# Performance work log

Hardware: AMD Instinct MI355X
Metric: run time of the kernel (lower is better)

The kernel has to match this reference:

```python
import jax, jax.numpy as jnp
import numpy as np

V, D, S, B, NL = 32000, 512, 1024, 2, 2
DS, KC, DI, DFF, E, TOPK = 16, 4, 1024, 2048, 8, 2
EPS = 1e-6


def rmsnorm(x, w):
    return x * jax.lax.rsqrt(jnp.mean(x * x, -1, keepdims=True) + EPS) * w


def mamba(x, in_w, conv_w, conv_b, x_proj_w, dt_w, dt_b, A_log, out_w):
    # x: (B, S, D)
    Bb, L, _ = x.shape
    xz = x @ in_w.T                      # (B, S, 2*DI)
    xi, z = jnp.split(xz, 2, axis=-1)    # each (B, S, DI)
    # causal depthwise conv (pad k-1 left == torch pad k-1 both + trim to L)
    xc = jnp.swapaxes(xi, 1, 2)          # (B, DI, S)
    xc = jax.lax.conv_general_dilated(
        xc, conv_w, window_strides=(1,), padding=[(KC - 1, 0)],
        dimension_numbers=("NCH", "OIH", "NCH"), feature_group_count=DI)
    xi = jnp.swapaxes(xc + conv_b[None, :, None], 1, 2)  # (B, S, DI)
    x_dbl = xi @ x_proj_w.T              # (B, S, 2*DS)
    B_param = x_dbl[..., DS:]            # (B, S, DS); first chunk overwritten in source
    delta = jax.nn.softplus(xi @ dt_w.T + dt_b)          # (B, S, DS)
    A = -jnp.exp(A_log)                  # (DI, DS)
    # recurrence coefficients (state dim summed out, as in source)
    a = jnp.exp(delta[:, :, None, :] * A[None, None]).sum(-1)        # (B, S, DI)
    b = xi * (delta * B_param).sum(-1, keepdims=True)                # (B, S, DI)

    def step(y, ab):
        at, bt = ab
        y = at * y + bt
        return y, y

    _, ys = jax.lax.scan(step, jnp.zeros((Bb, DI), x.dtype),
                         (jnp.swapaxes(a, 0, 1), jnp.swapaxes(b, 0, 1)))
    y = jnp.swapaxes(ys, 0, 1)           # (B, S, DI)
    y = y * jax.nn.silu(z)
    return y @ out_w.T                   # (B, S, D)


def moe(x, rw, rb, w1, b1, w2, b2):
    router_logits = x @ rw.T + rb                     # (B, S, E)
    probs = jax.nn.softmax(router_logits, axis=-1)
    topv, topi = jax.lax.top_k(probs, TOPK)
    wts = topv / topv.sum(-1, keepdims=True)          # renormalized gates
    h = jax.nn.gelu(jnp.einsum("bsd,efd->bsef", x, w1) + b1)   # (B, S, E, DFF)
    eo = jnp.einsum("bsef,edf->bsed", h, w2) + b2               # (B, S, E, D)
    sel = jnp.take_along_axis(eo, topi[..., None], axis=2)      # (B, S, K, D)
    out = (wts[..., None] * sel).sum(2)
    # load-balancing aux loss
    f = jax.nn.one_hot(topi, E).sum(2).mean((0, 1)) / TOPK
    P = probs.mean((0, 1))
    aux = E * jnp.sum(f * P)
    return out, aux


def setup_inputs() -> dict:
    key = jax.random.key(0)
    ks = jax.random.split(key, 16)
    f = lambda k, s: jax.random.normal(k, s, dtype=jnp.float32) * 0.02
    return {
        "input_ids": jax.random.randint(ks[0], (B, S), 0, V),
        "tok_emb": f(ks[1], (V, D)),
        "pos_emb": f(ks[2], (S, D)),
        "norm1_w": jnp.ones((NL, D), jnp.float32),
        "norm2_w": jnp.ones((NL, D), jnp.float32),
        "in_proj_w": f(ks[3], (NL, 2 * DI, D)),
        "conv_w": f(ks[4], (NL, DI, 1, KC)),
        "conv_b": jnp.zeros((NL, DI), jnp.float32),
        "x_proj_w": f(ks[5], (NL, 2 * DS, DI)),
        "dt_proj_w": f(ks[6], (NL, DS, DI)),
        "dt_proj_b": jnp.zeros((NL, DS), jnp.float32),
        "A_log": jnp.tile(jnp.log(jnp.arange(1, DS + 1, dtype=jnp.float32)), (NL, DI, 1)),
        "D_param": jnp.ones((NL, DI), jnp.float32),  # unused in forward, as in source
        "out_proj_w": f(ks[7], (NL, D, DI)),
        "router_w": f(ks[8], (NL, E, D)),
        "router_b": jnp.zeros((NL, E), jnp.float32),
        "w1": f(ks[9], (NL, E, DFF, D)),
        "b1": jnp.zeros((NL, E, DFF), jnp.float32),
        "w2": f(ks[10], (NL, E, D, DFF)),
        "b2": jnp.zeros((NL, E, D), jnp.float32),
        "final_norm_w": jnp.ones((D,), jnp.float32),
        "lm_head_w": f(ks[11], (V, D)),
    }


def reference(input_ids, tok_emb, pos_emb, norm1_w, norm2_w, in_proj_w, conv_w,
              conv_b, x_proj_w, dt_proj_w, dt_proj_b, A_log, D_param, out_proj_w,
              router_w, router_b, w1, b1, w2, b2, final_norm_w, lm_head_w):
    x = tok_emb[input_ids] + pos_emb[None, :, :]
    aux_total = jnp.zeros((), x.dtype)
    for l in range(NL):
        m = mamba(rmsnorm(x, norm1_w[l]), in_proj_w[l], conv_w[l], conv_b[l],
                  x_proj_w[l], dt_proj_w[l], dt_proj_b[l], A_log[l], out_proj_w[l])
        x = x + m
        ff, aux = moe(rmsnorm(x, norm2_w[l]), router_w[l], router_b[l],
                      w1[l], b1[l], w2[l], b2[l])
        x = x + ff
        aux_total = aux_total + aux
    x = rmsnorm(x, final_norm_w)
    logits = x @ lm_head_w.T
    return logits, aux_total
```

## Files before the change

kernel.cpp:

```cpp
#include <hip/hip_runtime.h>
#include <math.h>

#define S_    1024
#define D_    512
#define DI_   1024
#define DS_   16
#define KC_   4
#define E_    8
#define DFF_  2048
#define NTOK  2048
#define VOCAB 32000
#define NCHUNK 16
#define CHL    64
#define NSLOT 4096

typedef unsigned short ushort;
typedef unsigned int   uint;
typedef __attribute__((ext_vector_type(8))) short short8;
typedef __attribute__((ext_vector_type(4))) float f32x4;

__device__ __forceinline__ float gelu_sig(float x){
  float u = x*(1.5957691216057308f + 0.07135481627f*x*x);
  return x / (1.0f + expf(-u));
}
__device__ __forceinline__ ushort f2bf_rnd(float f){
  uint u = __float_as_uint(f);
  return (ushort)((u + 0x8000u) >> 16);
}
__device__ __forceinline__ float bf2f(ushort h){
  return __uint_as_float(((uint)h) << 16);
}
__device__ __forceinline__ void split1(float f, ushort& h, ushort& l){
  h = f2bf_rnd(f);
  float fh = bf2f(h);
  l = (ushort)(__float_as_uint(f - fh) >> 16);
}

__global__ __launch_bounds__(128) void k_embed(const int* __restrict__ ids,
    const float* __restrict__ tok, const float* __restrict__ pos, float* __restrict__ x){
  int t  = blockIdx.x;
  int d4 = threadIdx.x << 2;
  int s  = t & (S_-1);
  int id = ids[t];
  float4 tv = *(const float4*)(tok + (size_t)id*D_ + d4);
  float4 pv = *(const float4*)(pos + (size_t)s*D_ + d4);
  float4 o; o.x=tv.x+pv.x; o.y=tv.y+pv.y; o.z=tv.z+pv.z; o.w=tv.w+pv.w;
  *(float4*)(x + (size_t)t*D_ + d4) = o;
}

template<int ADD>
__global__ __launch_bounds__(128) void k_rmsnorm_split(float* __restrict__ x,
    const float* __restrict__ P3, const int* __restrict__ slotmap,
    const float* __restrict__ w, ushort* __restrict__ oh, ushort* __restrict__ ol){
  int t = blockIdx.x;
  int d4 = threadIdx.x << 2;
  float4 v = *(const float4*)(x + (size_t)t*D_ + d4);
  if (ADD){
    int s0 = slotmap[2*t], s1 = slotmap[2*t+1];
    #pragma unroll
    for (int ks=0; ks<4; ++ks){
      float4 p0 = *(const float4*)(P3 + ((size_t)ks*NSLOT + s0)*D_ + d4);
      float4 p1 = *(const float4*)(P3 + ((size_t)ks*NSLOT + s1)*D_ + d4);
      v.x += p0.x + p1.x; v.y += p0.y + p1.y; v.z += p0.z + p1.z; v.w += p0.w + p1.w;
    }
    *(float4*)(x + (size_t)t*D_ + d4) = v;
  }
  float ss = v.x*v.x + v.y*v.y + v.z*v.z + v.w*v.w;
  #pragma unroll
  for (int off=32; off>=1; off>>=1) ss += __shfl_down(ss, off);
  __shared__ float sred[2];
  if ((threadIdx.x & 63) == 0) sred[threadIdx.x >> 6] = ss;
  __syncthreads();
  float total = sred[0] + sred[1];
  float scale = 1.0f / sqrtf(total * (1.0f/D_) + 1e-6f);
  float4 wv = *(const float4*)(w + d4);
  float4 o; o.x=v.x*scale*wv.x; o.y=v.y*scale*wv.y; o.z=v.z*scale*wv.z; o.w=v.w*scale*wv.w;
  ushort h0,h1,h2,h3,l0,l1,l2,l3;
  split1(o.x,h0,l0); split1(o.y,h1,l1); split1(o.z,h2,l2); split1(o.w,h3,l3);
  *(uint2*)(oh + (size_t)t*D_ + d4) = make_uint2((uint)h0|((uint)h1<<16), (uint)h2|((uint)h3<<16));
  *(uint2*)(ol + (size_t)t*D_ + d4) = make_uint2((uint)l0|((uint)l1<<16), (uint)l2|((uint)l3<<16));
}

__global__ __launch_bounds__(128) void k_rmsnorm_router(float* __restrict__ x,
    const float* __restrict__ P2, const float* __restrict__ w,
    const float* __restrict__ rw, const float* __restrict__ rb,
    ushort* __restrict__ oh, ushort* __restrict__ ol,
    float* __restrict__ probs, float* __restrict__ topw, int* __restrict__ topi){
  int t = blockIdx.x;
  int tid = threadIdx.x;
  int d4 = tid << 2;
  float4 v = *(const float4*)(x + (size_t)t*D_ + d4);
  #pragma unroll
  for (int ks=0; ks<4; ++ks){
    float4 p = *(const float4*)(P2 + (size_t)ks*NTOK*D_ + (size_t)t*D_ + d4);
    v.x += p.x; v.y += p.y; v.z += p.z; v.w += p.w;
  }
  *(float4*)(x + (size_t)t*D_ + d4) = v;
  float ss = v.x*v.x + v.y*v.y + v.z*v.z + v.w*v.w;
  #pragma unroll
  for (int off=32; off>=1; off>>=1) ss += __shfl_down(ss, off);
  __shared__ float sred[2];
  __shared__ float lg2[2][E_];
  __shared__ float lg[E_];
  if ((tid & 63) == 0) sred[tid >> 6] = ss;
  __syncthreads();
  float total = sred[0] + sred[1];
  float scale = 1.0f / sqrtf(total * (1.0f/D_) + 1e-6f);
  float4 wv = *(const float4*)(w + d4);
  float4 o; o.x=v.x*scale*wv.x; o.y=v.y*scale*wv.y; o.z=v.z*scale*wv.z; o.w=v.w*scale*wv.w;
  ushort h0,h1,h2,h3,l0,l1,l2,l3;
  split1(o.x,h0,l0); split1(o.y,h1,l1); split1(o.z,h2,l2); split1(o.w,h3,l3);
  *(uint2*)(oh + (size_t)t*D_ + d4) = make_uint2((uint)h0|((uint)h1<<16), (uint)h2|((uint)h3<<16));
  *(uint2*)(ol + (size_t)t*D_ + d4) = make_uint2((uint)l0|((uint)l1<<16), (uint)l2|((uint)l3<<16));
  int lane = tid & 63, wid2 = tid >> 6;
  #pragma unroll
  for (int e=0;e<E_;e++){
    const float* rr = rw + (size_t)e*D_ + d4;
    float p = o.x*rr[0] + o.y*rr[1] + o.z*rr[2] + o.w*rr[3];
    #pragma unroll
    for (int off=32; off>=1; off>>=1) p += __shfl_down(p, off);
    if (lane==0) lg2[wid2][e] = p;
  }
  __syncthreads();
  if (tid==0){
    #pragma unroll
    for (int e=0;e<E_;e++) lg[e] = lg2[0][e] + lg2[1][e] + rb[e];
    float mx = lg[0];
    #pragma unroll
    for (int e=1;e<E_;e++) mx = fmaxf(mx, lg[e]);
    float pe[E_]; float sum = 0.f;
    #pragma unroll
    for (int e=0;e<E_;e++){ pe[e] = expf(lg[e]-mx); sum += pe[e]; }
    #pragma unroll
    for (int e=0;e<E_;e++){ pe[e] /= sum; probs[(size_t)t*E_ + e] = pe[e]; }
    int i1 = 0;
    #pragma unroll
    for (int e=1;e<E_;e++) if (pe[e] > pe[i1]) i1 = e;
    int i2 = (i1==0) ? 1 : 0;
    #pragma unroll
    for (int e=0;e<E_;e++) if (e!=i1 && pe[e] > pe[i2]) i2 = e;
    float wsum = pe[i1] + pe[i2];
    topw[t*2]   = pe[i1]/wsum;
    topw[t*2+1] = pe[i2]/wsum;
    topi[t*2] = i1; topi[t*2+1] = i2;
  }
}

__global__ __launch_bounds__(256) void k_split(const float* __restrict__ s,
    ushort* __restrict__ dh, ushort* __restrict__ dl, int n4){
  int i = blockIdx.x*256 + threadIdx.x;
  if (i >= n4) return;
  float4 v = ((const float4*)s)[i];
  ushort h0,h1,h2,h3,l0,l1,l2,l3;
  split1(v.x,h0,l0); split1(v.y,h1,l1); split1(v.z,h2,l2); split1(v.w,h3,l3);
  ((uint2*)dh)[i] = make_uint2((uint)h0|((uint)h1<<16), (uint)h2|((uint)h3<<16));
  ((uint2*)dl)[i] = make_uint2((uint)l0|((uint)l1<<16), (uint)l2|((uint)l3<<16));
}

__global__ __launch_bounds__(256) void k_bf16(const float* __restrict__ s,
    ushort* __restrict__ dh, int n4){
  int i = blockIdx.x*256 + threadIdx.x;
  if (i >= n4) return;
  float4 v = ((const float4*)s)[i];
  ushort h0 = f2bf_rnd(v.x), h1 = f2bf_rnd(v.y), h2 = f2bf_rnd(v.z), h3 = f2bf_rnd(v.w);
  ((uint2*)dh)[i] = make_uint2((uint)h0|((uint)h1<<16), (uint)h2|((uint)h3<<16));
}

template<int EPI, int NT, int KSP>
__global__ __launch_bounds__(256, 2) void gemm_mfma(
    const ushort* __restrict__ Ah, const ushort* __restrict__ Al,
    const ushort* __restrict__ Whb, const ushort* __restrict__ Wlb,
    float* __restrict__ Cb, ushort* __restrict__ Chh, ushort* __restrict__ Chl,
    const float* __restrict__ biasb, const float* __restrict__ slotw,
    const int* __restrict__ gidx, const int* __restrict__ offs,
    int M, int N, int K)
{
  int e, ks;
  if (KSP > 1){ e = blockIdx.z / KSP; ks = blockIdx.z % KSP; }
  else        { e = blockIdx.z;       ks = 0; }
  int off = 0, cnt = M;
  if (EPI==1 || EPI==3){
    off = offs[e];
    cnt = offs[e+1] - off;
    if ((int)(blockIdx.x*128) >= cnt) return;
  }
  const size_t wbase = (size_t)((EPI==1||EPI==3) ? e : 0) * N * K;
  const ushort* Wh = Whb + wbase;
  const ushort* Wl = Wlb + wbase;
  const float* bias = (EPI==1||EPI==3) ? (biasb + (size_t)e * N) : biasb;

  __shared__ ushort As_h[128][40];
  __shared__ ushort Ws_h[128][40];
  __shared__ ushort As_l[(NT>1)?128:1][40];
  __shared__ ushort Ws_l[(NT>1)?128:1][40];

  const int tid  = threadIdx.x;
  const int row0 = blockIdx.x * 128;
  const int col0 = blockIdx.y * 128;
  const int sr = tid >> 1;
  const int sh = (tid & 1) << 4;

  int aidx;
  if (EPI==1){ int lrr = row0 + sr; if (lrr > cnt-1) lrr = cnt-1; aidx = gidx[off + lrr]; }
  else if (EPI==3){ int lrr = row0 + sr; if (lrr > cnt-1) lrr = cnt-1; aidx = off + lrr; }
  else aidx = row0 + sr;
  const ushort* arh = Ah + (size_t)aidx*K;
  const ushort* arl = Al + (size_t)aidx*K;
  const ushort* wrh = Wh + (size_t)(col0 + sr)*K;
  const ushort* wrl = Wl + (size_t)(col0 + sr)*K;

  const int lane = tid & 63;
  const int wid  = tid >> 6;
  const int wrM  = (wid >> 1) * 64;
  const int wcN  = (wid & 1) * 64;
  const int lr   = lane & 15;
  const int kq   = lane >> 4;

  f32x4 zero = {0.f, 0.f, 0.f, 0.f};
  f32x4 acc[4][4];
  #pragma unroll
  for (int i=0;i<4;i++)
    #pragma unroll
    for (int j=0;j<4;j++) acc[i][j] = zero;

  const int k0 = ks * (K / KSP);
  const int k1 = k0 + (K / KSP);

  short8 rah[2], ral[2], rwh[2], rwl[2];
  rah[0]=*(const short8*)(arh+k0+sh); rah[1]=*(const short8*)(arh+k0+sh+8);
  rwh[0]=*(const short8*)(wrh+k0+sh); rwh[1]=*(const short8*)(wrh+k0+sh+8);
  if (NT>1){
    ral[0]=*(const short8*)(arl+k0+sh); ral[1]=*(const short8*)(arl+k0+sh+8);
    rwl[0]=*(const short8*)(wrl+k0+sh); rwl[1]=*(const short8*)(wrl+k0+sh+8);
  }

  for (int kk=k0; kk<k1; kk+=32){
    __syncthreads();
    *(short8*)&As_h[sr][sh]   = rah[0];  *(short8*)&As_h[sr][sh+8] = rah[1];
    *(short8*)&Ws_h[sr][sh]   = rwh[0];  *(short8*)&Ws_h[sr][sh+8] = rwh[1];
    if (NT>1){
      *(short8*)&As_l[sr][sh]   = ral[0];  *(short8*)&As_l[sr][sh+8] = ral[1];
      *(short8*)&Ws_l[sr][sh]   = rwl[0];  *(short8*)&Ws_l[sr][sh+8] = rwl[1];
    }
    if (kk + 32 < k1){
      int kn = kk + 32 + sh;
      rah[0]=*(const short8*)(arh+kn); rah[1]=*(const short8*)(arh+kn+8);
      rwh[0]=*(const short8*)(wrh+kn); rwh[1]=*(const short8*)(wrh+kn+8);
      if (NT>1){
        ral[0]=*(const short8*)(arl+kn); ral[1]=*(const short8*)(arl+kn+8);
        rwl[0]=*(const short8*)(wrl+kn); rwl[1]=*(const short8*)(wrl+kn+8);
      }
    }
    __syncthreads();

    short8 fah[4], fal[4], fbh[4], fbl[4];
    #pragma unroll
    for (int f=0; f<4; ++f){
      int rA = wrM + f*16 + lr;
      fah[f] = *(const short8*)&As_h[rA][kq*8];
      int rB = wcN + f*16 + lr;
      fbh[f] = *(const short8*)&Ws_h[rB][kq*8];
      if (NT>1){
        fal[f] = *(const short8*)&As_l[rA][kq*8];
        fbl[f] = *(const short8*)&Ws_l[rB][kq*8];
      }
    }
    #pragma unroll
    for (int i=0;i<4;i++)
      #pragma unroll
      for (int j=0;j<4;j++){
        f32x4 c = acc[i][j];
        if (NT==4) c = __builtin_amdgcn_mfma_f32_16x16x32_bf16(fal[i], fbl[j], c, 0,0,0);
        if (NT>1){
          c = __builtin_amdgcn_mfma_f32_16x16x32_bf16(fal[i], fbh[j], c, 0,0,0);
          c = __builtin_amdgcn_mfma_f32_16x16x32_bf16(fah[i], fbl[j], c, 0,0,0);
        }
        c = __builtin_amdgcn_mfma_f32_16x16x32_bf16(fah[i], fbh[j], c, 0,0,0);
        acc[i][j] = c;
      }
  }

  float bj[4];
  if (EPI==1 || EPI==3){
    #pragma unroll
    for (int j=0;j<4;j++) bj[j] = bias[col0 + wcN + j*16 + lr];
  }
  #pragma unroll
  for (int i=0;i<4;i++){
    #pragma unroll
    for (int jj=0;jj<4;jj++){
      int rt   = wrM + i*16 + kq*4 + jj;
      int grow = row0 + rt;
      if (EPI==0){
        float* cr = Cb + (size_t)grow*N + col0 + wcN + lr;
        #pragma unroll
        for (int j=0;j<4;j++) cr[j*16] = acc[i][j][jj];
      } else if (EPI==2){
        float* cr = Cb + (size_t)ks*M*N + (size_t)grow*N + col0 + wcN + lr;
        #pragma unroll
        for (int j=0;j<4;j++) cr[j*16] = acc[i][j][jj];
      } else if (EPI==1){
        if (grow < cnt){
          int slot = off + grow;
          size_t base = (size_t)slot*N + col0 + wcN + lr;
          #pragma unroll
          for (int j=0;j<4;j++){
            float g = gelu_sig(acc[i][j][jj] + bj[j]);
            ushort hh, ll; split1(g, hh, ll);
            Chh[base + j*16] = hh; Chl[base + j*16] = ll;
          }
        }
      } else {
        if (grow < cnt){
          int slot = off + grow;
          float sw = slotw[slot];
          float* cr = Cb + ((size_t)ks*NSLOT + slot)*N + col0 + wcN + lr;
          #pragma unroll
          for (int j=0;j<4;j++){
            float v = acc[i][j][jj];
            if (ks==0) v += bj[j];
            cr[j*16] = sw*v;
          }
        }
      }
    }
  }
}

__global__ __launch_bounds__(256) void k_convab(const float* __restrict__ xz,
    const float* __restrict__ cw, const float* __restrict__ cb,
    const float* __restrict__ xpw, const float* __restrict__ dtw,
    const float* __restrict__ dtb, const float* __restrict__ negA,
    float* __restrict__ a, float* __restrict__ bb){
  int t = blockIdx.x;
  int b = t >> 10, s = t & (S_-1);
  int tid = threadIdx.x;
  int c0 = tid << 2;
  __shared__ float xrow[DI_];
  __shared__ float outv[32];
  __shared__ float dl[DS_+1];
  float4 acc = *(const float4*)(cb + c0);
  #pragma unroll
  for (int k=0;k<KC_;k++){
    int ss = s - (KC_-1) + k;
    if (ss >= 0){
      float4 xv = *(const float4*)(xz + ((size_t)(b*S_+ss))*(2*DI_) + c0);
      acc.x += xv.x * cw[(c0+0)*KC_ + k];
      acc.y += xv.y * cw[(c0+1)*KC_ + k];
      acc.z += xv.z * cw[(c0+2)*KC_ + k];
      acc.w += xv.w * cw[(c0+3)*KC_ + k];
    }
  }
  *(float4*)(xrow + c0) = acc;
  __syncthreads();
  int wid = tid >> 6, lane = tid & 63;
  #pragma unroll
  for (int oi=0; oi<8; ++oi){
    int o = wid*8 + oi;
    const float* wr = (o < 16) ? (xpw + (size_t)(DS_ + o)*DI_) : (dtw + (size_t)(o-16)*DI_);
    float sum = 0.f;
    #pragma unroll
    for (int j=0;j<16;j++) sum += xrow[lane + 64*j] * wr[lane + 64*j];
    #pragma unroll
    for (int off=32; off>=1; off>>=1) sum += __shfl_down(sum, off);
    if (lane == 0) outv[o] = sum;
  }
  __syncthreads();
  if (tid < DS_){
    float d  = outv[16+tid] + dtb[tid];
    float sp = fmaxf(d, 0.f) + log1pf(expf(-fabsf(d)));
    dl[tid] = sp;
    float pr = sp * outv[tid];
    #pragma unroll
    for (int off=8; off>=1; off>>=1) pr += __shfl_down(pr, off);
    if (tid == 0) dl[DS_] = pr;
  }
  __syncthreads();
  float sdbv = dl[DS_];
  float av[4];
  #pragma unroll
  for (int i=0;i<4;i++){
    const float* nA = negA + (size_t)(c0+i)*DS_;
    float sum = 0.f;
    #pragma unroll
    for (int ds=0; ds<DS_; ds++) sum += expf(dl[ds] * nA[ds]);
    av[i] = sum;
  }
  *(float4*)(a + (size_t)t*DI_ + c0) = make_float4(av[0],av[1],av[2],av[3]);
  float4 bv; bv.x=acc.x*sdbv; bv.y=acc.y*sdbv; bv.z=acc.z*sdbv; bv.w=acc.w*sdbv;
  *(float4*)(bb + (size_t)t*DI_ + c0) = bv;
}

__global__ __launch_bounds__(256) void k_negA(const float* __restrict__ Alog, float* __restrict__ negA){
  int i = blockIdx.x*256 + threadIdx.x;
  negA[i] = -expf(Alog[i]);
}

__global__ __launch_bounds__(256) void k_scan1(const float* __restrict__ a,
    const float* __restrict__ bb, float* __restrict__ aprod, float* __restrict__ yend){
  int g  = blockIdx.x*256 + threadIdx.x;
  int di = g & (DI_-1);
  int c  = (g >> 10) & (NCHUNK-1);
  int b  = g >> 14;
  float ap = 1.f, y = 0.f;
  size_t base = ((size_t)b*S_ + (size_t)c*CHL)*DI_ + di;
  #pragma unroll 4
  for (int i=0;i<CHL;i++){
    float at = a[base + (size_t)i*DI_], bt = bb[base + (size_t)i*DI_];
    y = at*y + bt; ap *= at;
  }
  aprod[g] = ap; yend[g] = y;
}

__global__ __launch_bounds__(256) void k_scan2(const float* __restrict__ a,
    const float* __restrict__ bb, const float* __restrict__ xz,
    const float* __restrict__ aprod, const float* __restrict__ yend,
    ushort* __restrict__ yh, ushort* __restrict__ yl){
  int g  = blockIdx.x*256 + threadIdx.x;
  int di = g & (DI_-1);
  int c  = (g >> 10) & (NCHUNK-1);
  int b  = g >> 14;
  float y = 0.f;
  for (int j=0;j<c;j++){
    int gg = ((b*NCHUNK + j) << 10) + di;
    y = aprod[gg]*y + yend[gg];
  }
  size_t base = ((size_t)b*S_ + (size_t)c*CHL)*DI_ + di;
  #pragma unroll 4
  for (int i=0;i<CHL;i++){
    float at = a[base + (size_t)i*DI_], bt = bb[base + (size_t)i*DI_];
    y = at*y + bt;
    float z = xz[((size_t)(b*S_ + c*CHL + i))*(2*DI_) + DI_ + di];
    float sil = z / (1.f + expf(-z));
    float v = y * sil;
    ushort hh, ll; split1(v, hh, ll);
    yh[base + (size_t)i*DI_] = hh;
    yl[base + (size_t)i*DI_] = ll;
  }
}

__global__ __launch_bounds__(512) void k_compact_aux(const int* __restrict__ topi,
    const float* __restrict__ topw, const float* __restrict__ probs,
    int* __restrict__ gidx, float* __restrict__ asgw, int* __restrict__ slotmap,
    int* __restrict__ offs, float* __restrict__ dst, int first){
  int e = threadIdx.x >> 6, lane = threadIdx.x & 63;
  __shared__ int counts[E_];
  __shared__ float Psh[E_];
  int cnt = 0;
  for (int c=0; c<NTOK/64; ++c){
    int t = c*64 + lane;
    bool flag = (topi[2*t]==e) || (topi[2*t+1]==e);
    unsigned long long m = __ballot(flag);
    cnt += __popcll(m);
  }
  if (lane==0) counts[e] = cnt;
  __syncthreads();
  int base = 0;
  for (int i=0;i<e;i++) base += counts[i];
  if (lane==0) offs[e] = base;
  if (threadIdx.x==0){
    int tot=0;
    for (int i=0;i<E_;i++) tot += counts[i];
    offs[E_] = tot;
  }
  int run = base;
  for (int c=0; c<NTOK/64; ++c){
    int t = c*64 + lane;
    int which = (topi[2*t]==e) ? 0 : ((topi[2*t+1]==e) ? 1 : -1);
    bool flag = which >= 0;
    unsigned long long m = __ballot(flag);
    int rank = __popcll(m & ((1ull<<lane)-1ull));
    if (flag){
      int pos = run + rank;
      gidx[pos] = t;
      asgw[pos] = topw[2*t+which];
      slotmap[2*t+which] = pos;
    }
    run += __popcll(m);
  }
  float ps = 0.f;
  for (int c=0; c<NTOK/64; ++c){
    int t = c*64 + lane;
    ps += probs[(size_t)t*E_ + e];
  }
  #pragma unroll
  for (int off=32; off>=1; off>>=1) ps += __shfl_down(ps, off);
  if (lane==0) Psh[e] = ps;
  __syncthreads();
  if (threadIdx.x==0){
    float aux = 0.f;
    #pragma unroll
    for (int i=0;i<E_;i++){
      float P = Psh[i] * (1.0f/NTOK);
      float f = (float)counts[i] * (1.0f/(NTOK*2.0f));
      aux += f*P;
    }
    aux *= (float)E_;
    if (first) dst[0] = aux; else dst[0] += aux;
  }
}

extern "C" void kernel_launch(void* const* d_in, const int* in_sizes, int n_in,
                              void* d_out, int out_size, void* d_ws, size_t ws_size,
                              hipStream_t stream) {
  const int*   input_ids  = (const int*)  d_in[0];
  const float* tok_emb    = (const float*)d_in[1];
  const float* pos_emb    = (const float*)d_in[2];
  const float* norm1_w    = (const float*)d_in[3];
  const float* norm2_w    = (const float*)d_in[4];
  const float* in_proj_w  = (const float*)d_in[5];
  const float* conv_w     = (const float*)d_in[6];
  const float* conv_b     = (const float*)d_in[7];
  const float* x_proj_w   = (const float*)d_in[8];
  const float* dt_proj_w  = (const float*)d_in[9];
  const float* dt_proj_b  = (const float*)d_in[10];
  const float* A_log      = (const float*)d_in[11];
  const float* out_proj_w = (const float*)d_in[13];
  const float* router_w   = (const float*)d_in[14];
  const float* router_b   = (const float*)d_in[15];
  const float* w1         = (const float*)d_in[16];
  const float* b1         = (const float*)d_in[17];
  const float* w2         = (const float*)d_in[18];
  const float* b2         = (const float*)d_in[19];
  const float* final_norm = (const float*)d_in[20];
  const float* lm_head_w  = (const float*)d_in[21];
  float* out = (float*)d_out;

  float* f0 = (float*)d_ws;
  float*  x    = f0;
  ushort* xnh  = (ushort*)(f0 + 1048576);
  ushort* xnl  = xnh + 1048576;
  float*  xz   = f0 + 2097152;
  float*  a    = f0 + 6291456;
  float*  bb   = f0 + 8388608;
  ushort* yh   = (ushort*)(f0 + 10485760);
  ushort* yl   = yh + 2097152;
  float*  wsp  = f0 + 12582912;
  float*  P2   = f0 + 29360128;
  float*  P3   = f0 + 33554432;
  float*  negA = f0 + 41943040;
  float*  aprod= negA + 16384;
  float*  yendb= aprod + 32768;
  float*  probs= yendb + 32768;
  float*  topw = probs + 16384;
  float*  asgw = topw + 4096;
  int*    topi = (int*)(asgw + 4096);
  int*    gidx = topi + 4096;
  int*    slotmap = gidx + 4096;
  int*    offs = slotmap + 4096;

  ushort* hh  = (ushort*)xz;
  ushort* hl  = hh + 8388608;
  ushort* lmh = (ushort*)wsp;
  ushort* w1h = (ushort*)wsp;
  ushort* w1l = w1h + 8388608;
  ushort* w2h = w1l + 8388608;
  ushort* w2l = w2h + 8388608;
  ushort* wph = (ushort*)wsp;

  float* aux_dst = out + (size_t)NTOK*VOCAB;

  k_embed<<<NTOK, 128, 0, stream>>>(input_ids, tok_emb, pos_emb, x);

  for (int l=0; l<2; ++l){
    if (l == 0)
      k_rmsnorm_split<0><<<NTOK, 128, 0, stream>>>(x, nullptr, nullptr,
          norm1_w + (size_t)l*D_, xnh, xnl);
    else
      k_rmsnorm_split<1><<<NTOK, 128, 0, stream>>>(x, P3, slotmap,
          norm1_w + (size_t)l*D_, xnh, xnl);
    {
      int ne = 2*DI_*D_;
      ushort* wl_ = wph + ne;
      k_split<<<ne/1024, 256, 0, stream>>>(in_proj_w + (size_t)l*ne, wph, wl_, ne/4);
      gemm_mfma<0,3,1><<<dim3(16,16,1), 256, 0, stream>>>(xnh, xnl, wph, wl_,
          xz, nullptr, nullptr, nullptr, nullptr, nullptr, nullptr, NTOK, 2*DI_, D_);
    }
    k_negA<<<(DI_*DS_)/256, 256, 0, stream>>>(A_log + (size_t)l*DI_*DS_, negA);
    k_convab<<<NTOK, 256, 0, stream>>>(xz, conv_w + (size_t)l*DI_*KC_, conv_b + (size_t)l*DI_,
                                       x_proj_w + (size_t)l*2*DS_*DI_,
                                       dt_proj_w + (size_t)l*DS_*DI_, dt_proj_b + (size_t)l*DS_,
                                       negA, a, bb);
    k_scan1<<<(NTOK*NCHUNK)/256, 256, 0, stream>>>(a, bb, aprod, yendb);
    k_scan2<<<(NTOK*NCHUNK)/256, 256, 0, stream>>>(a, bb, xz, aprod, yendb, yh, yl);
    {
      int ne = D_*DI_;
      ushort* wl_ = wph + ne;
      k_split<<<ne/1024, 256, 0, stream>>>(out_proj_w + (size_t)l*ne, wph, wl_, ne/4);
      gemm_mfma<2,3,4><<<dim3(16,4,4), 256, 0, stream>>>(yh, yl, wph, wl_,
          P2, nullptr, nullptr, nullptr, nullptr, nullptr, nullptr, NTOK, D_, DI_);
    }
    k_rmsnorm_router<<<NTOK, 128, 0, stream>>>(x, P2, norm2_w + (size_t)l*D_,
        router_w + (size_t)l*E_*D_, router_b + (size_t)l*E_,
        xnh, xnl, probs, topw, topi);
    k_compact_aux<<<1, 512, 0, stream>>>(topi, topw, probs, gidx, asgw, slotmap, offs,
                                         aux_dst, l==0 ? 1 : 0);
    {
      int ne = E_*DFF_*D_;
      k_split<<<ne/1024, 256, 0, stream>>>(w1 + (size_t)l*ne, w1h, w1l, ne/4);
      k_split<<<ne/1024, 256, 0, stream>>>(w2 + (size_t)l*ne, w2h, w2l, ne/4);
      gemm_mfma<1,3,1><<<dim3(16,16,8), 256, 0, stream>>>(xnh, xnl, w1h, w1l,
          nullptr, hh, hl, b1 + (size_t)l*E_*DFF_, nullptr, gidx, offs, 0, DFF_, D_);
      gemm_mfma<3,3,4><<<dim3(16,4,32), 256, 0, stream>>>(hh, hl, w2h, w2l,
          P3, nullptr, nullptr, b2 + (size_t)l*E_*D_, asgw, gidx, offs, 0, D_, DFF_);
    }
  }

  k_rmsnorm_split<1><<<NTOK, 128, 0, stream>>>(x, P3, slotmap, final_norm, xnh, xnl);
  {
    int ne = VOCAB*D_;
    k_bf16<<<ne/1024, 256, 0, stream>>>(lm_head_w, lmh, ne/4);
    gemm_mfma<0,1,1><<<dim3(16,250,1), 256, 0, stream>>>(xnh, nullptr, lmh, nullptr,
        out, nullptr, nullptr, nullptr, nullptr, nullptr, nullptr, NTOK, VOCAB, D_);
  }
}
```

Before: 965.2 us.

## Batch all weight bf16 splits into one upfront kernel and stage compact_aux in LDS

```diff
diff --git a/kernel.cpp b/kernel.cpp
--- a/kernel.cpp
+++ b/kernel.cpp
@@ -19,6 +19,24 @@
 typedef __attribute__((ext_vector_type(8))) short short8;
 typedef __attribute__((ext_vector_type(4))) float f32x4;
 
+#define IN_US   0ull
+#define INL_US  1048576ull
+#define OUT_US  2097152ull
+#define OUTL_US 2621440ull
+#define W1_US   3145728ull
+#define W1L_US  11534336ull
+#define W2_US   19922944ull
+#define W2L_US  28311552ull
+#define LAYER_US 36700160ull
+#define LM_US   73400320ull
+#define IN4   262144
+#define OUT4  393216
+#define W14   2490368
+#define L4    4587520
+#define LM4   4096000
+#define LMEND 13271040
+#define TOT4  13279232
+
 __device__ __forceinline__ float gelu_sig(float x){
   float u = x*(1.5957691216057308f + 0.07135481627f*x*x);
   return x / (1.0f + expf(-u));
@@ -48,6 +66,55 @@
   *(float4*)(x + (size_t)t*D_ + d4) = o;
 }
 
+__global__ __launch_bounds__(256) void k_split_all(
+    const float* __restrict__ in_w, const float* __restrict__ out_w,
+    const float* __restrict__ w1, const float* __restrict__ w2,
+    const float* __restrict__ lm, const float* __restrict__ Alog,
+    ushort* __restrict__ wsp, float* __restrict__ negA){
+  int g = blockIdx.x*256 + threadIdx.x;
+  if (g >= TOT4) return;
+  if (g < 2*L4){
+    int l = (g < L4) ? 0 : 1;
+    int r = g - l*L4;
+    const float* src; size_t dh_off, dl_off;
+    if (r < IN4){
+      src = in_w + (size_t)l*1048576 + (size_t)r*4;
+      dh_off = (size_t)l*LAYER_US + IN_US  + (size_t)r*4;
+      dl_off = (size_t)l*LAYER_US + INL_US + (size_t)r*4;
+    } else if (r < OUT4){
+      int r2 = r - IN4;
+      src = out_w + (size_t)l*524288 + (size_t)r2*4;
+      dh_off = (size_t)l*LAYER_US + OUT_US  + (size_t)r2*4;
+      dl_off = (size_t)l*LAYER_US + OUTL_US + (size_t)r2*4;
+    } else if (r < W14){
+      int r3 = r - OUT4;
+      src = w1 + (size_t)l*8388608 + (size_t)r3*4;
+      dh_off = (size_t)l*LAYER_US + W1_US  + (size_t)r3*4;
+      dl_off = (size_t)l*LAYER_US + W1L_US + (size_t)r3*4;
+    } else {
+      int r4 = r - W14;
+      src = w2 + (size_t)l*8388608 + (size_t)r4*4;
+      dh_off = (size_t)l*LAYER_US + W2_US  + (size_t)r4*4;
+      dl_off = (size_t)l*LAYER_US + W2L_US + (size_t)r4*4;
+    }
+    float4 v = *(const float4*)src;
+    ushort h0,h1,h2,h3,l0,l1,l2,l3;
+    split1(v.x,h0,l0); split1(v.y,h1,l1); split1(v.z,h2,l2); split1(v.w,h3,l3);
+    *(uint2*)(wsp + dh_off) = make_uint2((uint)h0|((uint)h1<<16), (uint)h2|((uint)h3<<16));
+    *(uint2*)(wsp + dl_off) = make_uint2((uint)l0|((uint)l1<<16), (uint)l2|((uint)l3<<16));
+  } else if (g < LMEND){
+    int r = g - 2*L4;
+    float4 v = *(const float4*)(lm + (size_t)r*4);
+    ushort h0 = f2bf_rnd(v.x), h1 = f2bf_rnd(v.y), h2 = f2bf_rnd(v.z), h3 = f2bf_rnd(v.w);
+    *(uint2*)(wsp + LM_US + (size_t)r*4) = make_uint2((uint)h0|((uint)h1<<16), (uint)h2|((uint)h3<<16));
+  } else {
+    int r = g - LMEND;
+    float4 v = *(const float4*)(Alog + (size_t)r*4);
+    float4 o; o.x=-expf(v.x); o.y=-expf(v.y); o.z=-expf(v.z); o.w=-expf(v.w);
+    *(float4*)(negA + (size_t)r*4) = o;
+  }
+}
+
 template<int ADD>
 __global__ __launch_bounds__(128) void k_rmsnorm_split(float* __restrict__ x,
     const float* __restrict__ P3, const int* __restrict__ slotmap,
@@ -144,26 +211,6 @@
     topw[t*2+1] = pe[i2]/wsum;
     topi[t*2] = i1; topi[t*2+1] = i2;
   }
-}
-
-__global__ __launch_bounds__(256) void k_split(const float* __restrict__ s,
-    ushort* __restrict__ dh, ushort* __restrict__ dl, int n4){
-  int i = blockIdx.x*256 + threadIdx.x;
-  if (i >= n4) return;
-  float4 v = ((const float4*)s)[i];
-  ushort h0,h1,h2,h3,l0,l1,l2,l3;
-  split1(v.x,h0,l0); split1(v.y,h1,l1); split1(v.z,h2,l2); split1(v.w,h3,l3);
-  ((uint2*)dh)[i] = make_uint2((uint)h0|((uint)h1<<16), (uint)h2|((uint)h3<<16));
-  ((uint2*)dl)[i] = make_uint2((uint)l0|((uint)l1<<16), (uint)l2|((uint)l3<<16));
-}
-
-__global__ __launch_bounds__(256) void k_bf16(const float* __restrict__ s,
-    ushort* __restrict__ dh, int n4){
-  int i = blockIdx.x*256 + threadIdx.x;
-  if (i >= n4) return;
-  float4 v = ((const float4*)s)[i];
-  ushort h0 = f2bf_rnd(v.x), h1 = f2bf_rnd(v.y), h2 = f2bf_rnd(v.z), h3 = f2bf_rnd(v.w);
-  ((uint2*)dh)[i] = make_uint2((uint)h0|((uint)h1<<16), (uint)h2|((uint)h3<<16));
 }
 
 template<int EPI, int NT, int KSP>
@@ -391,11 +438,6 @@
   *(float4*)(bb + (size_t)t*DI_ + c0) = bv;
 }
 
-__global__ __launch_bounds__(256) void k_negA(const float* __restrict__ Alog, float* __restrict__ negA){
-  int i = blockIdx.x*256 + threadIdx.x;
-  negA[i] = -expf(Alog[i]);
-}
-
 __global__ __launch_bounds__(256) void k_scan1(const float* __restrict__ a,
     const float* __restrict__ bb, float* __restrict__ aprod, float* __restrict__ yend){
   int g  = blockIdx.x*256 + threadIdx.x;
@@ -443,13 +485,37 @@
     const float* __restrict__ topw, const float* __restrict__ probs,
     int* __restrict__ gidx, float* __restrict__ asgw, int* __restrict__ slotmap,
     int* __restrict__ offs, float* __restrict__ dst, int first){
-  int e = threadIdx.x >> 6, lane = threadIdx.x & 63;
+  int tid = threadIdx.x;
+  int e = tid >> 6, lane = tid & 63;
+  __shared__ unsigned char stop[NTOK*2];
+  __shared__ float stw[NTOK*2];
   __shared__ int counts[E_];
-  __shared__ float Psh[E_];
+  __shared__ float red[8][E_];
+  for (int i = tid; i < NTOK*2; i += 512){
+    stop[i] = (unsigned char)topi[i];
+    stw[i]  = topw[i];
+  }
+  float ps[E_];
+  #pragma unroll
+  for (int q=0;q<E_;q++) ps[q]=0.f;
+  for (int t = tid; t < NTOK; t += 512){
+    float4 p0 = *(const float4*)(probs + (size_t)t*E_);
+    float4 p1 = *(const float4*)(probs + (size_t)t*E_ + 4);
+    ps[0]+=p0.x; ps[1]+=p0.y; ps[2]+=p0.z; ps[3]+=p0.w;
+    ps[4]+=p1.x; ps[5]+=p1.y; ps[6]+=p1.z; ps[7]+=p1.w;
+  }
+  #pragma unroll
+  for (int q=0;q<E_;q++){
+    float v = ps[q];
+    #pragma unroll
+    for (int off=32; off>=1; off>>=1) v += __shfl_down(v, off);
+    if (lane==0) red[e][q] = v;
+  }
+  __syncthreads();
   int cnt = 0;
   for (int c=0; c<NTOK/64; ++c){
     int t = c*64 + lane;
-    bool flag = (topi[2*t]==e) || (topi[2*t+1]==e);
+    bool flag = (stop[2*t]==e) || (stop[2*t+1]==e);
     unsigned long long m = __ballot(flag);
     cnt += __popcll(m);
   }
@@ -458,7 +524,7 @@
   int base = 0;
   for (int i=0;i<e;i++) base += counts[i];
   if (lane==0) offs[e] = base;
-  if (threadIdx.x==0){
+  if (tid==0){
     int tot=0;
     for (int i=0;i<E_;i++) tot += counts[i];
     offs[E_] = tot;
@@ -466,32 +532,26 @@
   int run = base;
   for (int c=0; c<NTOK/64; ++c){
     int t = c*64 + lane;
-    int which = (topi[2*t]==e) ? 0 : ((topi[2*t+1]==e) ? 1 : -1);
+    int which = (stop[2*t]==e) ? 0 : ((stop[2*t+1]==e) ? 1 : -1);
     bool flag = which >= 0;
     unsigned long long m = __ballot(flag);
     int rank = __popcll(m & ((1ull<<lane)-1ull));
     if (flag){
       int pos = run + rank;
       gidx[pos] = t;
-      asgw[pos] = topw[2*t+which];
+      asgw[pos] = stw[2*t+which];
       slotmap[2*t+which] = pos;
     }
     run += __popcll(m);
   }
-  float ps = 0.f;
-  for (int c=0; c<NTOK/64; ++c){
-    int t = c*64 + lane;
-    ps += probs[(size_t)t*E_ + e];
-  }
-  #pragma unroll
-  for (int off=32; off>=1; off>>=1) ps += __shfl_down(ps, off);
-  if (lane==0) Psh[e] = ps;
-  __syncthreads();
-  if (threadIdx.x==0){
+  if (tid==0){
     float aux = 0.f;
     #pragma unroll
     for (int i=0;i<E_;i++){
-      float P = Psh[i] * (1.0f/NTOK);
+      float P = 0.f;
+      #pragma unroll
+      for (int wdd=0; wdd<8; ++wdd) P += red[wdd][i];
+      P *= (1.0f/NTOK);
       float f = (float)counts[i] * (1.0f/(NTOK*2.0f));
       aux += f*P;
     }
@@ -535,11 +595,13 @@
   float*  bb   = f0 + 8388608;
   ushort* yh   = (ushort*)(f0 + 10485760);
   ushort* yl   = yh + 2097152;
-  float*  wsp  = f0 + 12582912;
-  float*  P2   = f0 + 29360128;
-  float*  P3   = f0 + 33554432;
-  float*  negA = f0 + 41943040;
-  float*  aprod= negA + 16384;
+  ushort* hh   = (ushort*)(f0 + 12582912);
+  ushort* hl   = hh + 8388608;
+  float*  P2   = f0 + 20971520;
+  float*  P3   = f0 + 25165824;
+  ushort* wsplit = (ushort*)(f0 + 33554432);
+  float*  negA = f0 + 78446592;
+  float*  aprod= negA + 32768;
   float*  yendb= aprod + 32768;
   float*  probs= yendb + 32768;
   float*  topw = probs + 16384;
@@ -549,68 +611,42 @@
   int*    slotmap = gidx + 4096;
   int*    offs = slotmap + 4096;
 
-  ushort* hh  = (ushort*)xz;
-  ushort* hl  = hh + 8388608;
-  ushort* lmh = (ushort*)wsp;
-  ushort* w1h = (ushort*)wsp;
-  ushort* w1l = w1h + 8388608;
-  ushort* w2h = w1l + 8388608;
-  ushort* w2l = w2h + 8388608;
-  ushort* wph = (ushort*)wsp;
-
   float* aux_dst = out + (size_t)NTOK*VOCAB;
 
+  k_split_all<<<(TOT4+255)/256, 256, 0, stream>>>(in_proj_w, out_proj_w, w1, w2,
+                                                  lm_head_w, A_log, wsplit, negA);
   k_embed<<<NTOK, 128, 0, stream>>>(input_ids, tok_emb, pos_emb, x);
 
   for (int l=0; l<2; ++l){
+    ushort* L = wsplit + (size_t)l*LAYER_US;
     if (l == 0)
       k_rmsnorm_split<0><<<NTOK, 128, 0, stream>>>(x, nullptr, nullptr,
           norm1_w + (size_t)l*D_, xnh, xnl);
     else
       k_rmsnorm_split<1><<<NTOK, 128, 0, stream>>>(x, P3, slotmap,
           norm1_w + (size_t)l*D_, xnh, xnl);
-    {
-      int ne = 2*DI_*D_;
-      ushort* wl_ = wph + ne;
-      k_split<<<ne/1024, 256, 0, stream>>>(in_proj_w + (size_t)l*ne, wph, wl_, ne/4);
-      gemm_mfma<0,3,1><<<dim3(16,16,1), 256, 0, stream>>>(xnh, xnl, wph, wl_,
-          xz, nullptr, nullptr, nullptr, nullptr, nullptr, nullptr, NTOK, 2*DI_, D_);
-    }
-    k_negA<<<(DI_*DS_)/256, 256, 0, stream>>>(A_log + (size_t)l*DI_*DS_, negA);
+    gemm_mfma<0,3,1><<<dim3(16,16,1), 256, 0, stream>>>(xnh, xnl, L+IN_US, L+INL_US,
+        xz, nullptr, nullptr, nullptr, nullptr, nullptr, nullptr, NTOK, 2*DI_, D_);
     k_convab<<<NTOK, 256, 0, stream>>>(xz, conv_w + (size_t)l*DI_*KC_, conv_b + (size_t)l*DI_,
                                        x_proj_w + (size_t)l*2*DS_*DI_,
                                        dt_proj_w + (size_t)l*DS_*DI_, dt_proj_b + (size_t)l*DS_,
-                                       negA, a, bb);
+                                       negA + (size_t)l*DI_*DS_, a, bb);
     k_scan1<<<(NTOK*NCHUNK)/256, 256, 0, stream>>>(a, bb, aprod, yendb);
     k_scan2<<<(NTOK*NCHUNK)/256, 256, 0, stream>>>(a, bb, xz, aprod, yendb, yh, yl);
-    {
-      int ne = D_*DI_;
-      ushort* wl_ = wph + ne;
-      k_split<<<ne/1024, 256, 0, stream>>>(out_proj_w + (size_t)l*ne, wph, wl_, ne/4);
-      gemm_mfma<2,3,4><<<dim3(16,4,4), 256, 0, stream>>>(yh, yl, wph, wl_,
-          P2, nullptr, nullptr, nullptr, nullptr, nullptr, nullptr, NTOK, D_, DI_);
-    }
+    gemm_mfma<2,3,4><<<dim3(16,4,4), 256, 0, stream>>>(yh, yl, L+OUT_US, L+OUTL_US,
+        P2, nullptr, nullptr, nullptr, nullptr, nullptr, nullptr, NTOK, D_, DI_);
     k_rmsnorm_router<<<NTOK, 128, 0, stream>>>(x, P2, norm2_w + (size_t)l*D_,
         router_w + (size_t)l*E_*D_, router_b + (size_t)l*E_,
         xnh, xnl, probs, topw, topi);
     k_compact_aux<<<1, 512, 0, stream>>>(topi, topw, probs, gidx, asgw, slotmap, offs,
                                          aux_dst, l==0 ? 1 : 0);
-    {
-      int ne = E_*DFF_*D_;
-      k_split<<<ne/1024, 256, 0, stream>>>(w1 + (size_t)l*ne, w1h, w1l, ne/4);
-      k_split<<<ne/1024, 256, 0, stream>>>(w2 + (size_t)l*ne, w2h, w2l, ne/4);
-      gemm_mfma<1,3,1><<<dim3(16,16,8), 256, 0, stream>>>(xnh, xnl, w1h, w1l,
-          nullptr, hh, hl, b1 + (size_t)l*E_*DFF_, nullptr, gidx, offs, 0, DFF_, D_);
-      gemm_mfma<3,3,4><<<dim3(16,4,32), 256, 0, stream>>>(hh, hl, w2h, w2l,
-          P3, nullptr, nullptr, b2 + (size_t)l*E_*D_, asgw, gidx, offs, 0, D_, DFF_);
-    }
+    gemm_mfma<1,3,1><<<dim3(16,16,8), 256, 0, stream>>>(xnh, xnl, L+W1_US, L+W1L_US,
+        nullptr, hh, hl, b1 + (size_t)l*E_*DFF_, nullptr, gidx, offs, 0, DFF_, D_);
+    gemm_mfma<3,3,4><<<dim3(16,4,32), 256, 0, stream>>>(hh, hl, L+W2_US, L+W2L_US,
+        P3, nullptr, nullptr, b2 + (size_t)l*E_*D_, asgw, gidx, offs, 0, D_, DFF_);
   }
 
   k_rmsnorm_split<1><<<NTOK, 128, 0, stream>>>(x, P3, slotmap, final_norm, xnh, xnl);
-  {
-    int ne = VOCAB*D_;
-    k_bf16<<<ne/1024, 256, 0, stream>>>(lm_head_w, lmh, ne/4);
-    gemm_mfma<0,1,1><<<dim3(16,250,1), 256, 0, stream>>>(xnh, nullptr, lmh, nullptr,
-        out, nullptr, nullptr, nullptr, nullptr, nullptr, nullptr, NTOK, VOCAB, D_);
-  }
-}
+  gemm_mfma<0,1,1><<<dim3(16,250,1), 256, 0, stream>>>(xnh, nullptr, wsplit + LM_US, nullptr,
+      out, nullptr, nullptr, nullptr, nullptr, nullptr, nullptr, NTOK, VOCAB, D_);
+}
```

Measured after the change: 965.6 us. Within noise of the previous version (+0.0%).
